# Kernel tuning notes

Measured on AMD Instinct MI355X. Metric: run time of the kernel, lower is better.

## Reference

```python
import jax, jax.numpy as jnp
import numpy as np

FEAT_STRIDE = 16
PRE_NMS_TOP_N = 4000   # cfg[cfg_key].RPN_PRE_NMS_TOP_N
POST_NMS_TOP_N = 300   # cfg[cfg_key].RPN_POST_NMS_TOP_N
NMS_THRESH = 0.7       # cfg[cfg_key].RPN_NMS_THRESH


def _generate_anchors(base_size=16, ratios=(0.5, 1.0, 2.0), scales=(8, 16, 32)):
    ratios = np.array(ratios, dtype=np.float64)
    scales = np.array(scales, dtype=np.float64)
    base = np.array([1, 1, base_size, base_size], dtype=np.float64) - 1

    def whctrs(a):
        w = a[2] - a[0] + 1
        h = a[3] - a[1] + 1
        return w, h, a[0] + 0.5 * (w - 1), a[1] + 0.5 * (h - 1)

    def mk(ws, hs, xc, yc):
        ws = np.atleast_1d(ws)[:, None]
        hs = np.atleast_1d(hs)[:, None]
        return np.hstack((xc - 0.5 * (ws - 1), yc - 0.5 * (hs - 1),
                          xc + 0.5 * (ws - 1), yc + 0.5 * (hs - 1)))

    w, h, xc, yc = whctrs(base)
    size = w * h
    ws = np.round(np.sqrt(size / ratios))
    hs = np.round(ws * ratios)
    ratio_anchors = mk(ws, hs, xc, yc)
    out = []
    for i in range(ratio_anchors.shape[0]):
        w, h, xc, yc = whctrs(ratio_anchors[i])
        out.append(mk(w * scales, h * scales, xc, yc))
    return np.vstack(out).astype(np.float32)  # [9,4]


def _nms_keep(boxes, thresh):
    # boxes sorted by score desc, [N,4]; torchvision-style IoU (no +1).
    x1, y1, x2, y2 = boxes[:, 0], boxes[:, 1], boxes[:, 2], boxes[:, 3]
    areas = (x2 - x1) * (y2 - y1)
    lt = jnp.maximum(boxes[:, None, :2], boxes[None, :, :2])
    rb = jnp.minimum(boxes[:, None, 2:], boxes[None, :, 2:])
    wh = jnp.clip(rb - lt, 0.0)
    inter = wh[..., 0] * wh[..., 1]
    iou = inter / (areas[:, None] + areas[None, :] - inter + 1e-9)  # [N,N]
    N = boxes.shape[0]
    idx = jnp.arange(N)
    def body(i, keep):
        sup = (iou[i] > thresh) & (idx > i) & keep[i]
        return keep & ~sup
    return jax.lax.fori_loop(0, N, body, jnp.ones((N,), jnp.bool_))


def _per_image(boxes, scores):
    # pre-NMS top-k by score (matches sort-desc + slice)
    _, order = jax.lax.top_k(scores, PRE_NMS_TOP_N)
    b = boxes[order]
    keep = _nms_keep(jax.lax.stop_gradient(b), NMS_THRESH)
    rank = jnp.cumsum(keep) - 1                       # position among kept
    tgt = jnp.where(keep, rank, POST_NMS_TOP_N)       # OOB indices are dropped
    return jnp.zeros((POST_NMS_TOP_N, 4), boxes.dtype).at[tgt].set(b, mode='drop')


def reference(scores, bbox_deltas, im_info, anchors):
    B, A, H, W = scores.shape
    # anchor shifts over the feature grid
    sx = jnp.arange(W, dtype=scores.dtype) * FEAT_STRIDE
    sy = jnp.arange(H, dtype=scores.dtype) * FEAT_STRIDE
    yy, xx = jnp.meshgrid(sy, sx, indexing='ij')
    shifts = jnp.stack([xx.ravel(), yy.ravel(), xx.ravel(), yy.ravel()], axis=1)  # [K,4]
    all_anchors = (anchors[None, :, :] + shifts[:, None, :]).reshape(-1, 4)       # [K*A,4]

    deltas = bbox_deltas.transpose(0, 2, 3, 1).reshape(B, -1, 4)  # [B,K*A,4]
    sc = scores.transpose(0, 2, 3, 1).reshape(B, -1)              # [B,K*A]

    # bbox_transform_inv
    w = all_anchors[:, 2] - all_anchors[:, 0] + 1.0
    h = all_anchors[:, 3] - all_anchors[:, 1] + 1.0
    cx = all_anchors[:, 0] + 0.5 * w
    cy = all_anchors[:, 1] + 0.5 * h
    pcx = deltas[..., 0] * w + cx
    pcy = deltas[..., 1] * h + cy
    pw = jnp.exp(deltas[..., 2]) * w
    ph = jnp.exp(deltas[..., 3]) * h
    props = jnp.stack([pcx - 0.5 * pw, pcy - 0.5 * ph,
                       pcx + 0.5 * pw, pcy + 0.5 * ph], axis=-1)  # [B,K*A,4]

    # clip_boxes: x in [0, im_w-1], y in [0, im_h-1]
    hi = jnp.stack([im_info[:, 1] - 1, im_info[:, 0] - 1,
                    im_info[:, 1] - 1, im_info[:, 0] - 1], axis=1)  # [B,4]
    props = jnp.clip(props, 0.0, hi[:, None, :])

    boxes_out = jax.vmap(_per_image)(props, sc)  # [B,POST,4]
    batch_col = jnp.broadcast_to(
        jnp.arange(B, dtype=scores.dtype)[:, None, None], (B, POST_NMS_TOP_N, 1))
    return jnp.concatenate([batch_col, boxes_out], axis=-1)  # [B,POST,5]


def setup_inputs():
    key = jax.random.key(0)
    k1, k2 = jax.random.split(key)
    B, A, H, W = 4, 9, 50, 76
    scores = jax.random.normal(k1, (B, A, H, W), jnp.float32)
    bbox_deltas = jax.random.normal(k2, (B, 4 * A, H, W), jnp.float32) * 0.2
    im_info = jnp.tile(jnp.array([[800.0, 1216.0, 1.0]], jnp.float32), (B, 1))
    anchors = jnp.asarray(_generate_anchors())
    return {"scores": scores, "bbox_deltas": bbox_deltas,
            "im_info": im_info, "anchors": anchors}
```

## Files before the change

### kernel.cpp

```cpp
#include <hip/hip_runtime.h>
#include <stdint.h>

#define A_N 9
#define H_N 50
#define W_N 76
#define HW_N (H_N * W_N)
#define N_PROP (A_N * HW_N)
#define B_N 4
#define PRE_NMS 4000
#define POST_NMS 300
#define NMS_TH 0.7f
#define SORT_N 4096
#define MASK_WORDS 64
#define CAND_MAX 5120
#define NBINS 4096
#define NPAIR 32
#define NLW 5
#define DEC_BLKS ((N_PROP + 255) / 256)

__global__ __launch_bounds__(256) void decode_kernel(
    const float* __restrict__ scores,
    const float* __restrict__ deltas,
    const float* __restrict__ im_info,
    const float* __restrict__ anchors,
    float4* __restrict__ boxes,
    unsigned long long* __restrict__ keys) {
#pragma clang fp contract(off)
    int tid = threadIdx.x;
    int b = blockIdx.y;
    int r = blockIdx.x * 256 + tid;
    if (r >= N_PROP) return;

    int a = r / HW_N;
    int hw = r - a * HW_N;
    int hy = hw / W_N;
    int wx = hw - hy * W_N;

    float sx = (float)wx * 16.0f;
    float sy = (float)hy * 16.0f;
    float ax1 = anchors[a * 4 + 0] + sx;
    float ay1 = anchors[a * 4 + 1] + sy;
    float ax2 = anchors[a * 4 + 2] + sx;
    float ay2 = anchors[a * 4 + 3] + sy;
    float aw = ax2 - ax1 + 1.0f;
    float ah = ay2 - ay1 + 1.0f;
    float cx = ax1 + 0.5f * aw;
    float cy = ay1 + 0.5f * ah;

    const float* db = deltas + ((size_t)b * 36 + (size_t)a * 4) * HW_N + hw;
    float d0 = db[0];
    float d1 = db[HW_N];
    float d2 = db[2 * HW_N];
    float d3 = db[3 * HW_N];

    float pcx = d0 * aw + cx;
    float pcy = d1 * ah + cy;
    float pw  = expf(d2) * aw;
    float ph  = expf(d3) * ah;

    float x1 = pcx - 0.5f * pw;
    float y1 = pcy - 0.5f * ph;
    float x2 = pcx + 0.5f * pw;
    float y2 = pcy + 0.5f * ph;

    float xhi = im_info[b * 3 + 1] - 1.0f;
    float yhi = im_info[b * 3 + 0] - 1.0f;
    x1 = fminf(fmaxf(x1, 0.0f), xhi);
    y1 = fminf(fmaxf(y1, 0.0f), yhi);
    x2 = fminf(fmaxf(x2, 0.0f), xhi);
    y2 = fminf(fmaxf(y2, 0.0f), yhi);

    boxes[(size_t)b * N_PROP + r] = make_float4(x1, y1, x2, y2);

    float s = scores[((size_t)b * A_N + a) * HW_N + hw];
    unsigned f = __float_as_uint(s);
    unsigned sk = f ^ ((f & 0x80000000u) ? 0xFFFFFFFFu : 0x80000000u);
    unsigned n_ref = (unsigned)(hw * A_N + a);
    unsigned long long key = ((unsigned long long)sk << 32) | (unsigned)(~n_ref);
    keys[(size_t)b * N_PROP + r] = key;
}

__global__ __launch_bounds__(1024) void mid_kernel(
    const unsigned long long* __restrict__ keys,
    unsigned* __restrict__ cnt,
    unsigned long long* __restrict__ cand) {
    __shared__ unsigned hist[NBINS];
    __shared__ int Tlds;
    __shared__ unsigned cntL;
    const int b = blockIdx.x;
    const int tid = threadIdx.x;

    for (int i = tid; i < NBINS; i += 1024) hist[i] = 0u;
    if (tid == 0) cntL = 0u;
    __syncthreads();

    for (int it = 0; it < (N_PROP + 1023) / 1024; ++it) {
        int n = it * 1024 + tid;
        if (n < N_PROP) {
            unsigned long long k = keys[(size_t)b * N_PROP + n];
            atomicAdd(&hist[(unsigned)(k >> 52)], 1u);
        }
    }
    __syncthreads();

    if (tid < 64) {
        int lane = tid;
        unsigned gsum = 0;
        for (int j = 0; j < 64; ++j) gsum += hist[lane * 64 + j];
        unsigned s = gsum;
        for (int d = 1; d < 64; d <<= 1) {
            unsigned t = (unsigned)__shfl_down((int)s, d);
            if (lane + d < 64) s += t;
        }
        unsigned long long bal = __ballot(s >= PRE_NMS);
        int gstar = 63 - __builtin_clzll(bal);
        unsigned after = (gstar < 63)
            ? (unsigned)__builtin_amdgcn_readlane((int)s, gstar + 1) : 0u;
        unsigned R = PRE_NMS - after;
        unsigned s2 = hist[gstar * 64 + lane];
        for (int d = 1; d < 64; d <<= 1) {
            unsigned t = (unsigned)__shfl_down((int)s2, d);
            if (lane + d < 64) s2 += t;
        }
        unsigned long long bal2 = __ballot(s2 >= R);
        int j = 63 - __builtin_clzll(bal2);
        if (lane == 0) Tlds = gstar * 64 + j;
    }
    __syncthreads();

    const int Tb = Tlds;
    for (int it = 0; it < (N_PROP + 1023) / 1024; ++it) {
        int n = it * 1024 + tid;
        bool pred = false;
        unsigned long long k = 0ull;
        if (n < N_PROP) {
            k = keys[(size_t)b * N_PROP + n];
            pred = ((int)(unsigned)(k >> 52) >= Tb);
        }
        unsigned long long m = __ballot(pred);
        if (m) {
            int lane = tid & 63;
            int lead = __ffsll((unsigned long long)m) - 1;
            unsigned base = 0;
            if (lane == lead) base = atomicAdd(&cntL, (unsigned)__popcll(m));
            base = __shfl((int)base, lead);
            if (pred) {
                unsigned pos = base + (unsigned)__popcll(m & ((1ull << lane) - 1ull));
                if (pos < CAND_MAX) cand[(size_t)b * CAND_MAX + pos] = k;
            }
        }
    }
    __syncthreads();
    if (tid == 0) cnt[b] = cntL;
}

__global__ __launch_bounds__(256) void rank_scatter_kernel(
    const unsigned long long* __restrict__ cand,
    const unsigned* __restrict__ cnt,
    const float4* __restrict__ boxes,
    float4* __restrict__ sortedBoxes) {
    __shared__ unsigned long long sk[256];
    int b = blockIdx.y;
    int tid = threadIdx.x;
    int ci = blockIdx.x * 64 + (tid >> 2);
    int q = tid & 3;
    int mc = (int)min(cnt[b], (unsigned)CAND_MAX);
    unsigned long long my = (ci < mc) ? cand[(size_t)b * CAND_MAX + ci] : 0ull;
    int rank = 0;
    int nt = (mc + 255) >> 8;
    for (int t = 0; t < nt; ++t) {
        int j = t * 256 + tid;
        sk[tid] = (j < mc) ? cand[(size_t)b * CAND_MAX + j] : 0ull;
        __syncthreads();
#pragma unroll 16
        for (int c = 0; c < 64; ++c) {
            int cc = q * 64 + ((c + q * 17) & 63);
            rank += (sk[cc] > my) ? 1 : 0;
        }
        __syncthreads();
    }
    rank += __shfl_xor(rank, 1);
    rank += __shfl_xor(rank, 2);
    if (q == 0 && ci < mc && rank < PRE_NMS) {
        unsigned n_ref = ~(unsigned)(my & 0xFFFFFFFFull);
        unsigned a = n_ref % A_N;
        unsigned hw = n_ref / A_N;
        sortedBoxes[(size_t)b * SORT_N + rank] =
            boxes[(size_t)b * N_PROP + a * HW_N + hw];
    }
    if (q == 1) {
        int pi = blockIdx.x * 64 + (tid >> 2);
        if (pi >= PRE_NMS && pi < SORT_N)
            sortedBoxes[(size_t)b * SORT_N + pi] = make_float4(0.f, 0.f, 0.f, 0.f);
    }
}

__global__ __launch_bounds__(256) void iou_mask_kernel(
    const float4* __restrict__ sortedBoxes,
    unsigned long long* __restrict__ colmaj,
    unsigned long long* __restrict__ rowmaj) {
#pragma clang fp contract(off)
    int b = blockIdx.y;
    int wv = threadIdx.x >> 6;
    int t = threadIdx.x & 63;
    int k = blockIdx.x * 4 + wv;
    int rc = 0;
    while (k >= 64 - rc) { k -= 64 - rc; ++rc; }
    int cc = rc + k;

    __shared__ float4 colb[4][64];
    colb[wv][t] = sortedBoxes[(size_t)b * SORT_N + cc * 64 + t];
    __syncthreads();

    int r = rc * 64 + t;
    float4 rb = sortedBoxes[(size_t)b * SORT_N + r];
    float rarea = (rb.z - rb.x) * (rb.w - rb.y);
    unsigned long long word = 0ull;
    for (int c = 0; c < 64; ++c) {
        int j = cc * 64 + c;
        float4 cb = colb[wv][c];
        float carea = (cb.z - cb.x) * (cb.w - cb.y);
        float ltx = fmaxf(rb.x, cb.x);
        float lty = fmaxf(rb.y, cb.y);
        float rbx = fminf(rb.z, cb.z);
        float rby = fminf(rb.w, cb.w);
        float iw = fmaxf(rbx - ltx, 0.0f);
        float ih = fmaxf(rby - lty, 0.0f);
        float inter = iw * ih;
        float iou = inter / (rarea + carea - inter + 1e-9f);
        if (iou > NMS_TH && j > r) word |= (1ull << c);
    }
    colmaj[((size_t)b * MASK_WORDS + cc) * SORT_N + r] = word;
    rowmaj[((size_t)b * SORT_N + r) * MASK_WORDS + cc] = word;
}

__device__ __forceinline__ unsigned long long rl64(unsigned long long v, int src) {
    unsigned lo = (unsigned)__builtin_amdgcn_readlane((int)(unsigned)(v & 0xFFFFFFFFull), src);
    unsigned hi = (unsigned)__builtin_amdgcn_readlane((int)(unsigned)(v >> 32), src);
    return ((unsigned long long)hi << 32) | lo;
}

__device__ __forceinline__ unsigned long long redor64(unsigned long long alive,
                                                      unsigned long long v, int lane) {
    unsigned long long x = ((alive >> lane) & 1ull) ? v : 0ull;
    x |= __shfl_xor(x, 1);
    x |= __shfl_xor(x, 2);
    x |= __shfl_xor(x, 4);
    x |= __shfl_xor(x, 8);
    x |= __shfl_xor(x, 16);
    x |= __shfl_xor(x, 32);
    return x;
}

__device__ __forceinline__ void block_sync() {
    asm volatile("s_waitcnt lgkmcnt(0)" ::: "memory");
    __builtin_amdgcn_s_barrier();
    asm volatile("" ::: "memory");
}

#define GLOAD(dst, addr) \
    asm volatile("global_load_dwordx2 %0, %1, off" : "=v"(dst) : "v"(addr))
#define WAITV0 asm volatile("s_waitcnt vmcnt(0)" ::: "memory")
#define SCHED0 __builtin_amdgcn_sched_barrier(0)

#define TILE_COL(P, t) ((t) < 6 ? 2 * (P) + (t) : 2 * (P) + 1 + ((t) - 6))
#define TILE_RB(P, t)  ((size_t)((t) < 6 ? 2 * (P) : 2 * (P) + 1) << 6)
#define TILE_ADDR(P, t) \
    (C + (size_t)(TILE_COL(P, t) < 64 ? TILE_COL(P, t) : 63) * SORT_N + TILE_RB(P, t) + lane)

#define ISSUE_PAIR(P)                                                          \
    do {                                                                       \
        pf_vmask = 0u;                                                         \
        GLOAD(pf0,  TILE_ADDR(P, 0));  if (TILE_COL(P, 0)  < 64) pf_vmask |= 1u << 0;  \
        GLOAD(pf1,  TILE_ADDR(P, 1));  if (TILE_COL(P, 1)  < 64) pf_vmask |= 1u << 1;  \
        GLOAD(pf2,  TILE_ADDR(P, 2));  if (TILE_COL(P, 2)  < 64) pf_vmask |= 1u << 2;  \
        GLOAD(pf3,  TILE_ADDR(P, 3));  if (TILE_COL(P, 3)  < 64) pf_vmask |= 1u << 3;  \
        GLOAD(pf4,  TILE_ADDR(P, 4));  if (TILE_COL(P, 4)  < 64) pf_vmask |= 1u << 4;  \
        GLOAD(pf5,  TILE_ADDR(P, 5));  if (TILE_COL(P, 5)  < 64) pf_vmask |= 1u << 5;  \
        GLOAD(pf6,  TILE_ADDR(P, 6));  if (TILE_COL(P, 6)  < 64) pf_vmask |= 1u << 6;  \
        GLOAD(pf7,  TILE_ADDR(P, 7));  if (TILE_COL(P, 7)  < 64) pf_vmask |= 1u << 7;  \
        GLOAD(pf8,  TILE_ADDR(P, 8));  if (TILE_COL(P, 8)  < 64) pf_vmask |= 1u << 8;  \
        GLOAD(pf9,  TILE_ADDR(P, 9));  if (TILE_COL(P, 9)  < 64) pf_vmask |= 1u << 9;  \
        GLOAD(pf10, TILE_ADDR(P, 10)); if (TILE_COL(P, 10) < 64) pf_vmask |= 1u << 10; \
    } while (0)

#define NEXTROW2(rk)                                                           \
    int rk;                                                                    \
    {                                                                          \
        if (xA) { int bb_ = __builtin_ctzll(xA); xA &= xA - 1; rk = baseA + bb_; } \
        else if (xB) { int bb_ = __builtin_ctzll(xB); xB &= xB - 1; rk = baseB + bb_; } \
        else rk = rpad;                                                        \
    }

__global__ __launch_bounds__(512, 1) void nms_scan_kernel(
    const unsigned long long* __restrict__ colmaj,
    const unsigned long long* __restrict__ rowmaj,
    const float4* __restrict__ sortedBoxes,
    float* __restrict__ out) {
    int b = blockIdx.x;
    int tid = threadIdx.x;
    int lane = tid & 63;
    int wv = tid >> 6;
    const unsigned long long* C = colmaj + (size_t)b * MASK_WORDS * SORT_N;
    const unsigned long long* R = rowmaj + (size_t)b * SORT_N * MASK_WORDS;

    __shared__ int kept[POST_NMS];
    __shared__ unsigned remW[MASK_WORDS][2];
    __shared__ unsigned long long aliveLds[MASK_WORDS];
    __shared__ unsigned long long ring[4][11][64];
    __shared__ unsigned long long car2[2][2];
    __shared__ int doneLds;
    __shared__ int kcntLds;

    if (tid < MASK_WORDS) { remW[tid][0] = 0u; remW[tid][1] = 0u; aliveLds[tid] = 0ull; }
    if (tid < 4) car2[tid >> 1][tid & 1] = 0ull;
    if (tid == 0) { doneLds = 0; kcntLds = 0; }

    unsigned long long pf0=0,pf1=0,pf2=0,pf3=0,pf4=0,pf5=0,pf6=0,pf7=0,pf8=0,pf9=0,pf10=0;
    unsigned pf_vmask = 0u;
    bool pf_have = false;
    unsigned long long gp0=0,gp1=0,gp2=0,gp3=0,gp4=0,gp5=0,gp6=0,gp7=0;
    bool ld_valid = false;

    if (wv == 1) {
        for (int t = 0; t < 11; ++t) {
            int col = TILE_COL(0, t);
            unsigned long long v =
                (col < 64) ? C[(size_t)col * SORT_N + TILE_RB(0, t) + lane] : 0ull;
            ring[0][t][lane] = v;
        }
        ISSUE_PAIR(1);
        pf_have = true;
    }
    block_sync();

    unsigned long long carA = 0ull, carB = 0ull;
    int kcnt = 0;

    for (int q = 0; q < NPAIR; ++q) {
        if (wv == 0) {
            int A = 2 * q, Bg = A + 1, slot = q & 3;
            unsigned long long dA  = ring[slot][0][lane];
            unsigned long long tA1 = ring[slot][1][lane];
            unsigned long long tA2 = ring[slot][2][lane];
            unsigned long long tA3 = ring[slot][3][lane];
            unsigned long long dB  = ring[slot][6][lane];
            unsigned long long tB1 = ring[slot][7][lane];
            unsigned long long tB2 = ring[slot][8][lane];
            unsigned long long remA =
                ((unsigned long long)remW[A][1] << 32) | (unsigned long long)remW[A][0];
            unsigned long long remB =
                ((unsigned long long)remW[Bg][1] << 32) | (unsigned long long)remW[Bg][0];
            unsigned long long h2A = car2[q & 1][0];
            unsigned long long h2B = car2[q & 1][1];
            bool hit = false;
            unsigned long long aliveA = 0ull, aliveB = 0ull;
            unsigned long long pend = ~(remA | carA | h2A);
            while (pend) {
                int bit = __builtin_ctzll(pend);
                if (lane == 0) kept[kcnt] = (A << 6) + bit;
                ++kcnt;
                aliveA |= 1ull << bit;
                if (kcnt == POST_NMS) { hit = true; break; }
                pend &= ~(rl64(dA, bit) | (1ull << bit));
            }
            if (!hit) {
                unsigned long long nA1 = redor64(aliveA, tA1, lane);
                pend = ~(remB | carB | h2B | nA1);
                while (pend) {
                    int bit = __builtin_ctzll(pend);
                    if (lane == 0) kept[kcnt] = (Bg << 6) + bit;
                    ++kcnt;
                    aliveB |= 1ull << bit;
                    if (kcnt == POST_NMS) { hit = true; break; }
                    pend &= ~(rl64(dB, bit) | (1ull << bit));
                }
            }
            carA = redor64(aliveA, tA2, lane) | redor64(aliveB, tB1, lane);
            carB = redor64(aliveA, tA3, lane) | redor64(aliveB, tB2, lane);
            if (lane == 0) {
                aliveLds[A]  = aliveA;
                aliveLds[Bg] = aliveB;
                kcntLds = kcnt;
                if (hit) doneLds = 1;
            }
        } else if (wv == 1) {
            if (pf_have) {
                WAITV0;
                SCHED0;
                int wp = q + 1;
                if (wp < NPAIR) {
                    int ws = wp & 3;
                    ring[ws][0][lane]  = (pf_vmask & (1u << 0))  ? pf0  : 0ull;
                    ring[ws][1][lane]  = (pf_vmask & (1u << 1))  ? pf1  : 0ull;
                    ring[ws][2][lane]  = (pf_vmask & (1u << 2))  ? pf2  : 0ull;
                    ring[ws][3][lane]  = (pf_vmask & (1u << 3))  ? pf3  : 0ull;
                    ring[ws][4][lane]  = (pf_vmask & (1u << 4))  ? pf4  : 0ull;
                    ring[ws][5][lane]  = (pf_vmask & (1u << 5))  ? pf5  : 0ull;
                    ring[ws][6][lane]  = (pf_vmask & (1u << 6))  ? pf6  : 0ull;
                    ring[ws][7][lane]  = (pf_vmask & (1u << 7))  ? pf7  : 0ull;
                    ring[ws][8][lane]  = (pf_vmask & (1u << 8))  ? pf8  : 0ull;
                    ring[ws][9][lane]  = (pf_vmask & (1u << 9))  ? pf9  : 0ull;
                    ring[ws][10][lane] = (pf_vmask & (1u << 10)) ? pf10 : 0ull;
                }
                pf_have = false;
            }
            int ip = q + 2;
            if (ip < NPAIR) {
                ISSUE_PAIR(ip);
                pf_have = true;
            }
        } else if (wv == 2) {
            if (q >= 1) {
                int p = q - 1, sp = p & 3;
                unsigned long long aA = aliveLds[2 * p];
                unsigned long long aB = aliveLds[2 * p + 1];
                unsigned long long tA4 = ring[sp][4][lane];
                unsigned long long tA5 = ring[sp][5][lane];
                unsigned long long tB3 = ring[sp][9][lane];
                unsigned long long tB4 = ring[sp][10][lane];
                unsigned long long c0 = redor64(aA, tA4, lane) | redor64(aB, tB3, lane);
                unsigned long long c1 = redor64(aA, tA5, lane) | redor64(aB, tB4, lane);
                if (lane == 0) {
                    car2[(q + 1) & 1][0] = c0;
                    car2[(q + 1) & 1][1] = c1;
                }
            }
        } else {
            if (ld_valid) {
                WAITV0;
                SCHED0;
                unsigned long long acc =
                    ((gp0 | gp1) | (gp2 | gp3)) | ((gp4 | gp5) | (gp6 | gp7));
                unsigned lo = (unsigned)acc, hi = (unsigned)(acc >> 32);
                if (lo) atomicOr(&remW[lane][0], lo);
                if (hi) atomicOr(&remW[lane][1], hi);
                ld_valid = false;
            }
            if (q >= 1) {
                int p = q - 1, gA = 2 * p, gB = 2 * p + 1;
                unsigned long long aA = aliveLds[gA];
                unsigned long long aB = aliveLds[gB];
                int k = wv - 3;
                unsigned long long below = (1ull << lane) - 1ull;
                bool inA = (aA >> lane) & 1ull;
                bool inB = (aB >> lane) & 1ull;
                int posA = (int)__popcll(aA & below);
                int posB = (int)__popcll(aA) + (int)__popcll(aB & below);
                unsigned long long mA = __ballot(inA && (posA % NLW) == k);
                unsigned long long mB = __ballot(inB && (posB % NLW) == k);
                if (mA | mB) {
                    int baseA = gA << 6, baseB = gB << 6;
                    unsigned long long xA = mA, xB = mB;
                    int rpad = mA ? (baseA + __builtin_ctzll(mA))
                                  : (baseB + __builtin_ctzll(mB));
                    NEXTROW2(r0) NEXTROW2(r1) NEXTROW2(r2) NEXTROW2(r3)
                    NEXTROW2(r4) NEXTROW2(r5) NEXTROW2(r6) NEXTROW2(r7)
                    const unsigned long long* Rb = R + lane;
                    GLOAD(gp0, Rb + (size_t)r0 * MASK_WORDS);
                    GLOAD(gp1, Rb + (size_t)r1 * MASK_WORDS);
                    GLOAD(gp2, Rb + (size_t)r2 * MASK_WORDS);
                    GLOAD(gp3, Rb + (size_t)r3 * MASK_WORDS);
                    GLOAD(gp4, Rb + (size_t)r4 * MASK_WORDS);
                    GLOAD(gp5, Rb + (size_t)r5 * MASK_WORDS);
                    GLOAD(gp6, Rb + (size_t)r6 * MASK_WORDS);
                    GLOAD(gp7, Rb + (size_t)r7 * MASK_WORDS);
                    ld_valid = true;
                    unsigned long long ovf = 0ull;
                    while (xA) {
                        int bb = __builtin_ctzll(xA); xA &= xA - 1;
                        ovf |= Rb[(size_t)(baseA + bb) * MASK_WORDS];
                    }
                    while (xB) {
                        int bb = __builtin_ctzll(xB); xB &= xB - 1;
                        ovf |= Rb[(size_t)(baseB + bb) * MASK_WORDS];
                    }
                    if (ovf) {
                        unsigned lo = (unsigned)ovf, hi = (unsigned)(ovf >> 32);
                        if (lo) atomicOr(&remW[lane][0], lo);
                        if (hi) atomicOr(&remW[lane][1], hi);
                    }
                }
            }
        }
        block_sync();
        if (doneLds) break;
    }

    WAITV0;
    __syncthreads();

    int kc = kcntLds;
    for (int r = tid; r < POST_NMS; r += 512) {
        float* o = out + ((size_t)b * POST_NMS + r) * 5;
        float4 bx = make_float4(0.f, 0.f, 0.f, 0.f);
        if (r < kc) bx = sortedBoxes[(size_t)b * SORT_N + kept[r]];
        o[0] = (float)b;
        o[1] = bx.x;
        o[2] = bx.y;
        o[3] = bx.z;
        o[4] = bx.w;
    }
}

extern "C" void kernel_launch(void* const* d_in, const int* in_sizes, int n_in,
                              void* d_out, int out_size, void* d_ws, size_t ws_size,
                              hipStream_t stream) {
    const float* scores  = (const float*)d_in[0];
    const float* deltas  = (const float*)d_in[1];
    const float* im_info = (const float*)d_in[2];
    const float* anchors = (const float*)d_in[3];
    float* out = (float*)d_out;

    char* ws = (char*)d_ws;
    size_t off = 0;
    float4* boxes = (float4*)(ws + off);
    off += (size_t)B_N * N_PROP * sizeof(float4);
    off = (off + 255) & ~(size_t)255;
    unsigned long long* keys = (unsigned long long*)(ws + off);
    off += (size_t)B_N * N_PROP * sizeof(unsigned long long);
    off = (off + 255) & ~(size_t)255;
    float4* sortedBoxes = (float4*)(ws + off);
    off += (size_t)B_N * SORT_N * sizeof(float4);
    off = (off + 255) & ~(size_t)255;
    unsigned long long* colmaj = (unsigned long long*)(ws + off);
    off += (size_t)B_N * MASK_WORDS * SORT_N * sizeof(unsigned long long);
    off = (off + 255) & ~(size_t)255;
    unsigned long long* rowmaj = (unsigned long long*)(ws + off);
    off += (size_t)B_N * SORT_N * MASK_WORDS * sizeof(unsigned long long);
    off = (off + 255) & ~(size_t)255;
    unsigned long long* cand = (unsigned long long*)(ws + off);
    off += (size_t)B_N * CAND_MAX * sizeof(unsigned long long);
    off = (off + 255) & ~(size_t)255;
    unsigned* cnt = (unsigned*)(ws + off);
    off += (size_t)B_N * sizeof(unsigned);

    decode_kernel<<<dim3(DEC_BLKS, B_N), 256, 0, stream>>>(
        scores, deltas, im_info, anchors, boxes, keys);
    mid_kernel<<<B_N, 1024, 0, stream>>>(keys, cnt, cand);
    rank_scatter_kernel<<<dim3(CAND_MAX / 64, B_N), 256, 0, stream>>>(
        cand, cnt, boxes, sortedBoxes);
    iou_mask_kernel<<<dim3(520, B_N), 256, 0, stream>>>(sortedBoxes, colmaj, rowmaj);
    nms_scan_kernel<<<B_N, 512, 0, stream>>>(colmaj, rowmaj, sortedBoxes, out);
}
```

Measured before the change: 203.5 us.

## Store transposed near-diagonal IoU tiles and use ballots instead of shuffle reductions

The IoU mask kernel now also writes a transposed copy of the tiles within six column-blocks of the diagonal, built with 64 ballots per wave. The NMS scan reads these transposed tiles and replaces the readlane and six-step shuffle OR-reductions with a single ballot of (tile & alive) != 0. This shortens the serial dependency chain in the single-block-per-image scan, at the cost of extra ballot work and stores in the IoU kernel. The column-major mask is still written even though the scan no longer reads it.

Result: no change. 199.7 us (-1.9%).

```diff
diff --git a/kernel.cpp b/kernel.cpp
--- a/kernel.cpp
+++ b/kernel.cpp
@@ -16,6 +16,7 @@
 #define NBINS 4096
 #define NPAIR 32
 #define NLW 5
+#define NDELTA 6
 #define DEC_BLKS ((N_PROP + 255) / 256)
 
 __global__ __launch_bounds__(256) void decode_kernel(
@@ -198,7 +199,8 @@
 __global__ __launch_bounds__(256) void iou_mask_kernel(
     const float4* __restrict__ sortedBoxes,
     unsigned long long* __restrict__ colmaj,
-    unsigned long long* __restrict__ rowmaj) {
+    unsigned long long* __restrict__ rowmaj,
+    unsigned long long* __restrict__ trans) {
 #pragma clang fp contract(off)
     int b = blockIdx.y;
     int wv = threadIdx.x >> 6;
@@ -232,24 +234,21 @@
     }
     colmaj[((size_t)b * MASK_WORDS + cc) * SORT_N + r] = word;
     rowmaj[((size_t)b * SORT_N + r) * MASK_WORDS + cc] = word;
-}
-
-__device__ __forceinline__ unsigned long long rl64(unsigned long long v, int src) {
-    unsigned lo = (unsigned)__builtin_amdgcn_readlane((int)(unsigned)(v & 0xFFFFFFFFull), src);
-    unsigned hi = (unsigned)__builtin_amdgcn_readlane((int)(unsigned)(v >> 32), src);
-    return ((unsigned long long)hi << 32) | lo;
-}
-
-__device__ __forceinline__ unsigned long long redor64(unsigned long long alive,
-                                                      unsigned long long v, int lane) {
-    unsigned long long x = ((alive >> lane) & 1ull) ? v : 0ull;
-    x |= __shfl_xor(x, 1);
-    x |= __shfl_xor(x, 2);
-    x |= __shfl_xor(x, 4);
-    x |= __shfl_xor(x, 8);
-    x |= __shfl_xor(x, 16);
-    x |= __shfl_xor(x, 32);
-    return x;
+
+    int delta = cc - rc;
+    if (delta < NDELTA) {
+        unsigned long long tw = 0ull;
+        for (int j = 0; j < 64; ++j) {
+            unsigned long long bal = __ballot(((word >> j) & 1ull) != 0ull);
+            if (t == j) tw = bal;
+        }
+        trans[(((size_t)b * MASK_WORDS + rc) * NDELTA + delta) * 64 + t] = tw;
+    }
+}
+
+__device__ __forceinline__ unsigned long long bal_nz(unsigned long long tileT,
+                                                     unsigned long long alive) {
+    return __ballot((tileT & alive) != 0ull);
 }
 
 __device__ __forceinline__ void block_sync() {
@@ -263,25 +262,26 @@
 #define WAITV0 asm volatile("s_waitcnt vmcnt(0)" ::: "memory")
 #define SCHED0 __builtin_amdgcn_sched_barrier(0)
 
-#define TILE_COL(P, t) ((t) < 6 ? 2 * (P) + (t) : 2 * (P) + 1 + ((t) - 6))
-#define TILE_RB(P, t)  ((size_t)((t) < 6 ? 2 * (P) : 2 * (P) + 1) << 6)
-#define TILE_ADDR(P, t) \
-    (C + (size_t)(TILE_COL(P, t) < 64 ? TILE_COL(P, t) : 63) * SORT_N + TILE_RB(P, t) + lane)
+#define TRG(P, t)  ((t) < 6 ? 2 * (P) : 2 * (P) + 1)
+#define TRD(P, t)  ((t) < 6 ? (t) : (t) - 6)
+#define TRVAL(P, t) (TRG(P, t) + TRD(P, t) < 64)
+#define TR_ADDR(P, t) \
+    (TR + (((size_t)TRG(P, t) * NDELTA + (TRVAL(P, t) ? TRD(P, t) : 0)) << 6) + lane)
 
 #define ISSUE_PAIR(P)                                                          \
     do {                                                                       \
         pf_vmask = 0u;                                                         \
-        GLOAD(pf0,  TILE_ADDR(P, 0));  if (TILE_COL(P, 0)  < 64) pf_vmask |= 1u << 0;  \
-        GLOAD(pf1,  TILE_ADDR(P, 1));  if (TILE_COL(P, 1)  < 64) pf_vmask |= 1u << 1;  \
-        GLOAD(pf2,  TILE_ADDR(P, 2));  if (TILE_COL(P, 2)  < 64) pf_vmask |= 1u << 2;  \
-        GLOAD(pf3,  TILE_ADDR(P, 3));  if (TILE_COL(P, 3)  < 64) pf_vmask |= 1u << 3;  \
-        GLOAD(pf4,  TILE_ADDR(P, 4));  if (TILE_COL(P, 4)  < 64) pf_vmask |= 1u << 4;  \
-        GLOAD(pf5,  TILE_ADDR(P, 5));  if (TILE_COL(P, 5)  < 64) pf_vmask |= 1u << 5;  \
-        GLOAD(pf6,  TILE_ADDR(P, 6));  if (TILE_COL(P, 6)  < 64) pf_vmask |= 1u << 6;  \
-        GLOAD(pf7,  TILE_ADDR(P, 7));  if (TILE_COL(P, 7)  < 64) pf_vmask |= 1u << 7;  \
-        GLOAD(pf8,  TILE_ADDR(P, 8));  if (TILE_COL(P, 8)  < 64) pf_vmask |= 1u << 8;  \
-        GLOAD(pf9,  TILE_ADDR(P, 9));  if (TILE_COL(P, 9)  < 64) pf_vmask |= 1u << 9;  \
-        GLOAD(pf10, TILE_ADDR(P, 10)); if (TILE_COL(P, 10) < 64) pf_vmask |= 1u << 10; \
+        GLOAD(pf0,  TR_ADDR(P, 0));  if (TRVAL(P, 0))  pf_vmask |= 1u << 0;    \
+        GLOAD(pf1,  TR_ADDR(P, 1));  if (TRVAL(P, 1))  pf_vmask |= 1u << 1;    \
+        GLOAD(pf2,  TR_ADDR(P, 2));  if (TRVAL(P, 2))  pf_vmask |= 1u << 2;    \
+        GLOAD(pf3,  TR_ADDR(P, 3));  if (TRVAL(P, 3))  pf_vmask |= 1u << 3;    \
+        GLOAD(pf4,  TR_ADDR(P, 4));  if (TRVAL(P, 4))  pf_vmask |= 1u << 4;    \
+        GLOAD(pf5,  TR_ADDR(P, 5));  if (TRVAL(P, 5))  pf_vmask |= 1u << 5;    \
+        GLOAD(pf6,  TR_ADDR(P, 6));  if (TRVAL(P, 6))  pf_vmask |= 1u << 6;    \
+        GLOAD(pf7,  TR_ADDR(P, 7));  if (TRVAL(P, 7))  pf_vmask |= 1u << 7;    \
+        GLOAD(pf8,  TR_ADDR(P, 8));  if (TRVAL(P, 8))  pf_vmask |= 1u << 8;    \
+        GLOAD(pf9,  TR_ADDR(P, 9));  if (TRVAL(P, 9))  pf_vmask |= 1u << 9;    \
+        GLOAD(pf10, TR_ADDR(P, 10)); if (TRVAL(P, 10)) pf_vmask |= 1u << 10;   \
     } while (0)
 
 #define NEXTROW2(rk)                                                           \
@@ -293,7 +293,7 @@
     }
 
 __global__ __launch_bounds__(512, 1) void nms_scan_kernel(
-    const unsigned long long* __restrict__ colmaj,
+    const unsigned long long* __restrict__ trans,
     const unsigned long long* __restrict__ rowmaj,
     const float4* __restrict__ sortedBoxes,
     float* __restrict__ out) {
@@ -301,7 +301,7 @@
     int tid = threadIdx.x;
     int lane = tid & 63;
     int wv = tid >> 6;
-    const unsigned long long* C = colmaj + (size_t)b * MASK_WORDS * SORT_N;
+    const unsigned long long* TR = trans + (size_t)b * MASK_WORDS * NDELTA * 64;
     const unsigned long long* R = rowmaj + (size_t)b * SORT_N * MASK_WORDS;
 
     __shared__ int kept[POST_NMS];
@@ -324,9 +324,8 @@
 
     if (wv == 1) {
         for (int t = 0; t < 11; ++t) {
-            int col = TILE_COL(0, t);
-            unsigned long long v =
-                (col < 64) ? C[(size_t)col * SORT_N + TILE_RB(0, t) + lane] : 0ull;
+            unsigned long long v = TRVAL(0, t)
+                ? TR[(((size_t)TRG(0, t)) * NDELTA + TRD(0, t)) * 64 + lane] : 0ull;
             ring[0][t][lane] = v;
         }
         ISSUE_PAIR(1);
@@ -362,10 +361,11 @@
                 ++kcnt;
                 aliveA |= 1ull << bit;
                 if (kcnt == POST_NMS) { hit = true; break; }
-                pend &= ~(rl64(dA, bit) | (1ull << bit));
+                unsigned long long d = __ballot(((dA >> bit) & 1ull) != 0ull);
+                pend &= ~(d | (1ull << bit));
             }
             if (!hit) {
-                unsigned long long nA1 = redor64(aliveA, tA1, lane);
+                unsigned long long nA1 = bal_nz(tA1, aliveA);
                 pend = ~(remB | carB | h2B | nA1);
                 while (pend) {
                     int bit = __builtin_ctzll(pend);
@@ -373,11 +373,12 @@
                     ++kcnt;
                     aliveB |= 1ull << bit;
                     if (kcnt == POST_NMS) { hit = true; break; }
-                    pend &= ~(rl64(dB, bit) | (1ull << bit));
+                    unsigned long long d = __ballot(((dB >> bit) & 1ull) != 0ull);
+                    pend &= ~(d | (1ull << bit));
                 }
             }
-            carA = redor64(aliveA, tA2, lane) | redor64(aliveB, tB1, lane);
-            carB = redor64(aliveA, tA3, lane) | redor64(aliveB, tB2, lane);
+            carA = bal_nz(tA2, aliveA) | bal_nz(tB1, aliveB);
+            carB = bal_nz(tA3, aliveA) | bal_nz(tB2, aliveB);
             if (lane == 0) {
                 aliveLds[A]  = aliveA;
                 aliveLds[Bg] = aliveB;
@@ -419,8 +420,8 @@
                 unsigned long long tA5 = ring[sp][5][lane];
                 unsigned long long tB3 = ring[sp][9][lane];
                 unsigned long long tB4 = ring[sp][10][lane];
-                unsigned long long c0 = redor64(aA, tA4, lane) | redor64(aB, tB3, lane);
-                unsigned long long c1 = redor64(aA, tA5, lane) | redor64(aB, tB4, lane);
+                unsigned long long c0 = bal_nz(tA4, aA) | bal_nz(tB3, aB);
+                unsigned long long c1 = bal_nz(tA5, aA) | bal_nz(tB4, aB);
                 if (lane == 0) {
                     car2[(q + 1) & 1][0] = c0;
                     car2[(q + 1) & 1][1] = c1;
@@ -529,6 +530,9 @@
     unsigned long long* rowmaj = (unsigned long long*)(ws + off);
     off += (size_t)B_N * SORT_N * MASK_WORDS * sizeof(unsigned long long);
     off = (off + 255) & ~(size_t)255;
+    unsigned long long* trans = (unsigned long long*)(ws + off);
+    off += (size_t)B_N * MASK_WORDS * NDELTA * 64 * sizeof(unsigned long long);
+    off = (off + 255) & ~(size_t)255;
     unsigned long long* cand = (unsigned long long*)(ws + off);
     off += (size_t)B_N * CAND_MAX * sizeof(unsigned long long);
     off = (off + 255) & ~(size_t)255;
@@ -540,6 +544,7 @@
     mid_kernel<<<B_N, 1024, 0, stream>>>(keys, cnt, cand);
     rank_scatter_kernel<<<dim3(CAND_MAX / 64, B_N), 256, 0, stream>>>(
         cand, cnt, boxes, sortedBoxes);
-    iou_mask_kernel<<<dim3(520, B_N), 256, 0, stream>>>(sortedBoxes, colmaj, rowmaj);
-    nms_scan_kernel<<<B_N, 512, 0, stream>>>(colmaj, rowmaj, sortedBoxes, out);
-}
+    iou_mask_kernel<<<dim3(520, B_N), 256, 0, stream>>>(
+        sortedBoxes, colmaj, rowmaj, trans);
+    nms_scan_kernel<<<B_N, 512, 0, stream>>>(trans, rowmaj, sortedBoxes, out);
+}
```
